# Kernel tuning notes

Hardware: AMD Instinct MI355X
Metric: run time of the kernel (lower is better)

The kernel has to match this reference:

```python
import jax, jax.numpy as jnp
import numpy as np

IN_F = 4096      # in_features (d_model)
OUT_F = 16384    # out_features (4*d_model FFN)
N_TOK = 8192     # tokens = batch*seq
K = OUT_F // 2   # number of kept output rows (static for jit)


def setup_inputs() -> dict:
    key = jax.random.key(0)
    k1, k2, k3, k4 = jax.random.split(key, 4)
    data = jax.random.normal(k1, (N_TOK, IN_F), jnp.float32)
    weight = jax.random.normal(k2, (OUT_F, IN_F), jnp.float32) * 0.02
    bias = jax.random.normal(k3, (OUT_F,), jnp.float32) * 0.02
    # mask with exactly K ones at random positions (static count -> jit-safe)
    perm = jax.random.permutation(k4, OUT_F)
    mask = jnp.zeros((OUT_F,), jnp.int32).at[perm[:K]].set(1)
    return {"data": data, "weight": weight, "bias": bias, "mask": mask}


def reference(data, weight, bias, mask):
    # mask.nonzero()[0] -> selected output-feature indices (ascending, as torch)
    idx = jnp.nonzero(mask, size=K)[0]                 # [K]
    w_sel = jnp.take(weight, idx, axis=0)              # [K, IN_F] row gather
    b_sel = jnp.take(bias, idx, axis=0)                # [K]
    # F.linear: data @ w_sel^T + b_sel  -> [N_TOK, K]
    return jnp.einsum('ti,ki->tk', data, w_sel) + b_sel
```

## Files before the change

kernel.cpp:

```cpp
#include <hip/hip_runtime.h>
#include <hip/hip_bf16.h>

typedef __bf16 bf16_t;
typedef __attribute__((ext_vector_type(8))) __bf16 bf16x8;
typedef __attribute__((ext_vector_type(4))) float f32x4;

constexpr int IN_F  = 4096;
constexpr int OUT_F = 16384;
constexpr int N_TOK = 8192;
constexpr int KSEL  = 8192;
constexpr long A_ELEMS = (long)N_TOK * IN_F;

constexpr int BM = 256, BN = 256, BK = 64;
constexpr int NT = IN_F / BK;

#define GLOBAL_CAST(p) (const __attribute__((address_space(1))) void*)(p)
#define LDS_CAST(p)    (__attribute__((address_space(3))) void*)(p)

__global__ __launch_bounds__(1024) void build_idx_kernel(
    const int* __restrict__ mask, const float* __restrict__ bias,
    int* __restrict__ idx, float* __restrict__ bsel)
{
    const int t    = threadIdx.x;
    const int lane = t & 63;
    const int wave = t >> 6;
    const int base_i = t * 16;

    int m[16];
    const int4* mp = (const int4*)(mask + base_i);
#pragma unroll
    for (int v = 0; v < 4; ++v) {
        int4 q = mp[v];
        m[v*4+0] = q.x; m[v*4+1] = q.y; m[v*4+2] = q.z; m[v*4+3] = q.w;
    }
    int cnt = 0;
#pragma unroll
    for (int j = 0; j < 16; ++j) cnt += (m[j] != 0) ? 1 : 0;

    int incl = cnt;
#pragma unroll
    for (int d = 1; d < 64; d <<= 1) {
        int o = __shfl_up(incl, (unsigned)d);
        if (lane >= d) incl += o;
    }

    __shared__ int wsum[16];
    __shared__ int wbase[16];
    if (lane == 63) wsum[wave] = incl;
    __syncthreads();
    if (t == 0) {
        int s = 0;
        for (int w = 0; w < 16; ++w) { wbase[w] = s; s += wsum[w]; }
    }
    __syncthreads();

    int p = wbase[wave] + (incl - cnt);
#pragma unroll
    for (int j = 0; j < 16; ++j) {
        if (m[j]) {
            int i = base_i + j;
            idx[p]  = i;
            bsel[p] = bias[i];
            ++p;
        }
    }
}

__global__ __launch_bounds__(256) void convert_kernel(
    const float* __restrict__ A, const float* __restrict__ W,
    const int* __restrict__ idx,
    bf16_t* __restrict__ Ab, bf16_t* __restrict__ Wb)
{
    const long nvecA = A_ELEMS / 8;
    const long total = nvecA * 2;
    const long stride = (long)gridDim.x * blockDim.x;
    for (long v = (long)blockIdx.x * blockDim.x + threadIdx.x; v < total; v += stride) {
        const float4* src;
        bf16_t* dst;
        if (v < nvecA) {
            src = (const float4*)(A + v * 8);
            dst = Ab + v * 8;
        } else {
            long u = v - nvecA;
            int j = (int)(u >> 9);
            int k = (int)(u & 511) * 8;
            src = (const float4*)(W + (long)idx[j] * IN_F + k);
            dst = Wb + u * 8;
        }
        float4 x = src[0], y = src[1];
        bf16x8 o;
        o[0]=(bf16_t)x.x; o[1]=(bf16_t)x.y; o[2]=(bf16_t)x.z; o[3]=(bf16_t)x.w;
        o[4]=(bf16_t)y.x; o[5]=(bf16_t)y.y; o[6]=(bf16_t)y.z; o[7]=(bf16_t)y.w;
        *(bf16x8*)dst = o;
    }
}

__global__ __launch_bounds__(512, 2) void gemm8p_kernel(
    const bf16_t* __restrict__ A, const bf16_t* __restrict__ B,
    const float* __restrict__ bsel, float* __restrict__ C)
{
    __shared__ __attribute__((aligned(16))) char lds[131072];

    const int tid  = threadIdx.x;
    const int w    = tid >> 6;
    const int lane = tid & 63;
    const int wr   = w >> 2;
    const int wc   = w & 3;

    const int bid = blockIdx.x;
    const int swz = (bid & 7) * 128 + (bid >> 3);
    const int m0 = (swz & 31) * BM;
    const int n0 = (swz >> 5) * BN;

    const int pr  = lane >> 3;
    const int csw = ((lane & 7) ^ pr) * 8;
    const bf16_t* aSrc[2][2];
    const bf16_t* bSrc[2][2];
#pragma unroll
    for (int h = 0; h < 2; ++h)
#pragma unroll
        for (int j = 0; j < 2; ++j) {
            const int row = h * 128 + (w * 2 + j) * 8 + pr;
            aSrc[h][j] = A + (long)(m0 + row) * IN_F + csw;
            bSrc[h][j] = B + (long)(n0 + row) * IN_F + csw;
        }

#define ST_A(buf, h, tl) do {                                                  \
    __builtin_amdgcn_global_load_lds(GLOBAL_CAST(aSrc[h][0] + (long)(tl)*BK),  \
        LDS_CAST(lds + (buf)*65536 + (h)*16384 + w*2048), 16, 0, 0);           \
    __builtin_amdgcn_global_load_lds(GLOBAL_CAST(aSrc[h][1] + (long)(tl)*BK),  \
        LDS_CAST(lds + (buf)*65536 + (h)*16384 + w*2048 + 1024), 16, 0, 0);    \
} while (0)
#define ST_B(buf, h, tl) do {                                                  \
    __builtin_amdgcn_global_load_lds(GLOBAL_CAST(bSrc[h][0] + (long)(tl)*BK),  \
        LDS_CAST(lds + (buf)*65536 + 32768 + (h)*16384 + w*2048), 16, 0, 0);   \
    __builtin_amdgcn_global_load_lds(GLOBAL_CAST(bSrc[h][1] + (long)(tl)*BK),  \
        LDS_CAST(lds + (buf)*65536 + 32768 + (h)*16384 + w*2048 + 1024),       \
        16, 0, 0);                                                             \
} while (0)

    f32x4 acc[8][4];
#pragma unroll
    for (int m = 0; m < 8; ++m)
#pragma unroll
        for (int n = 0; n < 4; ++n)
#pragma unroll
            for (int j = 0; j < 4; ++j) acc[m][n][j] = 0.f;

    const int fr    = lane & 15;
    const int kslot = lane >> 4;
    const int sp0b = ((kslot       ^ (fr & 7)) << 4);
    const int sp1b = (((4 + kslot) ^ (fr & 7)) << 4);

    const int a0s0 = wr * 16384 + fr * 128 + sp0b;
    const int a0s1 = wr * 16384 + fr * 128 + sp1b;
    const int a1s0 = a0s0 + 65536;
    const int a1s1 = a0s1 + 65536;
    const int bbase = 32768 + (wc >> 1) * 16384 + ((wc & 1) * 64 + fr) * 128;
    const int b0s0 = bbase + sp0b;
    const int b0s1 = bbase + sp1b;
    const int b1s0 = b0s0 + 65536;
    const int b1s1 = b0s1 + 65536;

    bf16x8 af[4][2], bg[4][2];

#define RDA(s0, s1, mq) do {                                                   \
    _Pragma("unroll") for (int mm = 0; mm < 4; ++mm) {                         \
        af[mm][0] = *(const bf16x8*)(lds + (s0) + (mq)*8192 + mm*2048);        \
        af[mm][1] = *(const bf16x8*)(lds + (s1) + (mq)*8192 + mm*2048);        \
    } } while (0)
#define RDB(s0, s1, nh) do {                                                   \
    _Pragma("unroll") for (int nn = 0; nn < 2; ++nn) {                         \
        bg[(nh)*2+nn][0] = *(const bf16x8*)(lds + (s0) + ((nh)*2+nn)*2048);    \
        bg[(nh)*2+nn][1] = *(const bf16x8*)(lds + (s1) + ((nh)*2+nn)*2048);    \
    } } while (0)
#define MFMAQ(mq, nh) do {                                                     \
    __builtin_amdgcn_s_setprio(1);                                             \
    _Pragma("unroll") for (int mm = 0; mm < 4; ++mm)                           \
    _Pragma("unroll") for (int nn = 0; nn < 2; ++nn) {                         \
        const int m = (mq) * 4 + mm, n = (nh) * 2 + nn;                        \
        acc[m][n] = __builtin_amdgcn_mfma_f32_16x16x32_bf16(                   \
            af[mm][0], bg[n][0], acc[m][n], 0, 0, 0);                          \
        acc[m][n] = __builtin_amdgcn_mfma_f32_16x16x32_bf16(                   \
            af[mm][1], bg[n][1], acc[m][n], 0, 0, 0);                          \
    }                                                                          \
    __builtin_amdgcn_s_setprio(0); } while (0)
#define BAR()    __builtin_amdgcn_s_barrier()
#define LGKM0()  asm volatile("s_waitcnt lgkmcnt(0)" ::: "memory")
#define LGKMH()  asm volatile("s_waitcnt lgkmcnt(8)" ::: "memory")
#define VMC8()   asm volatile("s_waitcnt vmcnt(8)" ::: "memory")
#define VMC0()   asm volatile("s_waitcnt vmcnt(0)" ::: "memory")

    ST_A(0, 0, 0); ST_A(0, 1, 0); ST_B(0, 0, 0); ST_B(0, 1, 0);
    ST_A(1, 0, 1); ST_A(1, 1, 1); ST_B(1, 0, 1); ST_B(1, 1, 1);
    VMC8(); BAR();

    for (int I = 0; I < NT / 2; ++I) {
        const int t = 2 * I, u = t + 1;
        const bool s2 = (I < NT / 2 - 1);

        RDA(a0s0, a0s1, 0); RDB(b0s0, b0s1, 0);
        LGKMH(); BAR(); LGKM0(); MFMAQ(0, 0); BAR();
        RDB(b0s0, b0s1, 1);
        BAR(); LGKM0(); MFMAQ(0, 1); BAR();
        RDA(a0s0, a0s1, 1);
        if (s2) { ST_B(0, 0, t + 2); ST_B(0, 1, t + 2); }
        BAR(); LGKM0(); MFMAQ(1, 0); BAR();
        if (s2) { ST_A(0, 0, t + 2); ST_A(0, 1, t + 2); }
        BAR(); MFMAQ(1, 1); if (s2) VMC8(); else VMC0(); BAR();
        RDA(a1s0, a1s1, 0); RDB(b1s0, b1s1, 0);
        LGKMH(); BAR(); LGKM0(); MFMAQ(0, 0); BAR();
        RDB(b1s0, b1s1, 1);
        BAR(); LGKM0(); MFMAQ(0, 1); BAR();
        RDA(a1s0, a1s1, 1);
        if (s2) { ST_B(1, 0, u + 2); ST_B(1, 1, u + 2); }
        BAR(); LGKM0(); MFMAQ(1, 0); BAR();
        if (s2) { ST_A(1, 0, u + 2); ST_A(1, 1, u + 2); }
        BAR(); MFMAQ(1, 1); if (s2) VMC8(); else VMC0(); BAR();
    }
    VMC0();

#undef ST_A
#undef ST_B
#undef RDA
#undef RDB
#undef MFMAQ
#undef BAR
#undef LGKM0
#undef LGKMH
#undef VMC8
#undef VMC0

    float b4[4];
#pragma unroll
    for (int n = 0; n < 4; ++n) b4[n] = bsel[n0 + wc * 64 + n * 16 + fr];

    const int rbase = m0 + wr * 128 + kslot * 4;
#pragma unroll
    for (int m = 0; m < 8; ++m)
#pragma unroll
        for (int n = 0; n < 4; ++n) {
            const int col = n0 + wc * 64 + n * 16 + fr;
#pragma unroll
            for (int j = 0; j < 4; ++j)
                C[(long)(rbase + m * 16 + j) * KSEL + col] = acc[m][n][j] + b4[n];
        }
}

__global__ __launch_bounds__(256) void gemm_f32staged_kernel(
    const float* __restrict__ A, const float* __restrict__ W,
    const int* __restrict__ idx, const float* __restrict__ bsel,
    float* __restrict__ C)
{
    constexpr int FBM = 128, FBN = 128, BK2 = 32;
    __shared__ __attribute__((aligned(16))) float Asf[FBM * BK2];
    __shared__ __attribute__((aligned(16))) float Bsf[FBN * BK2];

    const int tid  = threadIdx.x;
    const int wave = tid >> 6;
    const int lane = tid & 63;
    const int wrf  = wave >> 1;
    const int wcf  = wave & 1;

    const int m0 = blockIdx.x * FBM;
    const int n0 = blockIdx.y * FBN;

    const int srow = lane >> 3;
    const int scol = (lane & 7) * 4;

    const float* aptr[4];
    const float* bptr[4];
#pragma unroll
    for (int i = 0; i < 4; ++i) {
        aptr[i] = A + (long)(m0 + wave * 32 + i * 8 + srow) * IN_F + scol;
        const int br = idx[n0 + wave * 32 + i * 8 + srow];
        bptr[i] = W + (long)br * IN_F + scol;
    }

    f32x4 acc[4][4];
#pragma unroll
    for (int m = 0; m < 4; ++m)
#pragma unroll
        for (int n = 0; n < 4; ++n)
#pragma unroll
            for (int j = 0; j < 4; ++j) acc[m][n][j] = 0.f;

    const int fr = lane & 15;
    const int fk = (lane >> 4) * 8;

    for (int k0 = 0; k0 < IN_F; k0 += BK2) {
#pragma unroll
        for (int i = 0; i < 4; ++i) {
            __builtin_amdgcn_global_load_lds(GLOBAL_CAST(aptr[i] + k0),
                LDS_CAST(&Asf[(wave * 32 + i * 8) * BK2]), 16, 0, 0);
            __builtin_amdgcn_global_load_lds(GLOBAL_CAST(bptr[i] + k0),
                LDS_CAST(&Bsf[(wave * 32 + i * 8) * BK2]), 16, 0, 0);
        }
        __syncthreads();

        bf16x8 af[4], bg[4];
#pragma unroll
        for (int m = 0; m < 4; ++m) {
            const float* p = &Asf[(wrf * 64 + m * 16 + fr) * BK2 + fk];
            f32x4 x = *(const f32x4*)p, y = *(const f32x4*)(p + 4);
#pragma unroll
            for (int j = 0; j < 4; ++j) { af[m][j] = (bf16_t)x[j]; af[m][4+j] = (bf16_t)y[j]; }
        }
#pragma unroll
        for (int n = 0; n < 4; ++n) {
            const float* p = &Bsf[(wcf * 64 + n * 16 + fr) * BK2 + fk];
            f32x4 x = *(const f32x4*)p, y = *(const f32x4*)(p + 4);
#pragma unroll
            for (int j = 0; j < 4; ++j) { bg[n][j] = (bf16_t)x[j]; bg[n][4+j] = (bf16_t)y[j]; }
        }
#pragma unroll
        for (int m = 0; m < 4; ++m)
#pragma unroll
            for (int n = 0; n < 4; ++n)
                acc[m][n] = __builtin_amdgcn_mfma_f32_16x16x32_bf16(
                    af[m], bg[n], acc[m][n], 0, 0, 0);
        __syncthreads();
    }

    float b4[4];
#pragma unroll
    for (int n = 0; n < 4; ++n) b4[n] = bsel[n0 + wcf * 64 + n * 16 + fr];

    const int rbase = m0 + wrf * 64 + (lane >> 4) * 4;
#pragma unroll
    for (int m = 0; m < 4; ++m)
#pragma unroll
        for (int n = 0; n < 4; ++n) {
            const int col = n0 + wcf * 64 + n * 16 + fr;
#pragma unroll
            for (int j = 0; j < 4; ++j)
                C[(long)(rbase + m * 16 + j) * KSEL + col] = acc[m][n][j] + b4[n];
        }
}

extern "C" void kernel_launch(void* const* d_in, const int* in_sizes, int n_in,
                              void* d_out, int out_size, void* d_ws, size_t ws_size,
                              hipStream_t stream)
{
    const float* data   = (const float*)d_in[0];
    const float* weight = (const float*)d_in[1];
    const float* bias   = (const float*)d_in[2];
    const int*   mask   = (const int*)d_in[3];
    float*       out    = (float*)d_out;

    char* ws = (char*)d_ws;
    int*   idx  = (int*)ws;
    float* bsel = (float*)(ws + (KSEL * 4));
    bf16_t* Ab  = (bf16_t*)(ws + (KSEL * 8));
    bf16_t* Wb  = Ab + A_ELEMS;

    const size_t NEED = (size_t)KSEL * 8 + (size_t)A_ELEMS * 2 * 2;

    build_idx_kernel<<<1, 1024, 0, stream>>>(mask, bias, idx, bsel);

    if (ws_size >= NEED) {
        convert_kernel<<<2048, 256, 0, stream>>>(data, weight, idx, Ab, Wb);
        gemm8p_kernel<<<1024, 512, 0, stream>>>(Ab, Wb, bsel, out);
    } else {
        dim3 grid(N_TOK / 128, KSEL / 128);
        gemm_f32staged_kernel<<<grid, 256, 0, stream>>>(data, weight, idx, bsel, out);
    }
}
```

Baseline: 686.7 us.

## Double-buffer LDS fragment registers to overlap reads with MFMA and halve barriers

Splits the A and B register fragments into two sets so that the LDS reads for the next quarter-tile are issued while MFMAs on the current set run. The number of barriers per k-step drops from about two per quarter to one, and the global-load waits are adjusted to vmcnt(4). Register pressure goes up, which can lower occupancy or cause spills. The reworked wait and barrier ordering also carries a risk of LDS read/write races.

```diff
diff --git a/kernel.cpp b/kernel.cpp
--- a/kernel.cpp
+++ b/kernel.cpp
@@ -156,78 +156,107 @@
     const int a0s1 = wr * 16384 + fr * 128 + sp1b;
     const int a1s0 = a0s0 + 65536;
     const int a1s1 = a0s1 + 65536;
-    const int bbase = 32768 + (wc >> 1) * 16384 + ((wc & 1) * 64 + fr) * 128;
-    const int b0s0 = bbase + sp0b;
-    const int b0s1 = bbase + sp1b;
+    const int bb   = 32768 + (wc >> 1) * 16384 + ((wc & 1) * 64 + fr) * 128;
+    const int b0s0 = bb + sp0b;
+    const int b0s1 = bb + sp1b;
     const int b1s0 = b0s0 + 65536;
     const int b1s1 = b0s1 + 65536;
 
-    bf16x8 af[4][2], bg[4][2];
-
-#define RDA(s0, s1, mq) do {                                                   \
+    bf16x8 afA[4][2], afB[4][2], bg0[2][2], bg1[2][2];
+
+#define RDA_TO(DST, s0, s1, mq) do {                                           \
     _Pragma("unroll") for (int mm = 0; mm < 4; ++mm) {                         \
-        af[mm][0] = *(const bf16x8*)(lds + (s0) + (mq)*8192 + mm*2048);        \
-        af[mm][1] = *(const bf16x8*)(lds + (s1) + (mq)*8192 + mm*2048);        \
+        DST[mm][0] = *(const bf16x8*)(lds + (s0) + (mq)*8192 + mm*2048);       \
+        DST[mm][1] = *(const bf16x8*)(lds + (s1) + (mq)*8192 + mm*2048);       \
     } } while (0)
-#define RDB(s0, s1, nh) do {                                                   \
+#define RDB_TO(DST, s0, s1, nh) do {                                           \
     _Pragma("unroll") for (int nn = 0; nn < 2; ++nn) {                         \
-        bg[(nh)*2+nn][0] = *(const bf16x8*)(lds + (s0) + ((nh)*2+nn)*2048);    \
-        bg[(nh)*2+nn][1] = *(const bf16x8*)(lds + (s1) + ((nh)*2+nn)*2048);    \
+        DST[nn][0] = *(const bf16x8*)(lds + (s0) + ((nh)*2+nn)*2048);          \
+        DST[nn][1] = *(const bf16x8*)(lds + (s1) + ((nh)*2+nn)*2048);          \
     } } while (0)
-#define MFMAQ(mq, nh) do {                                                     \
+#define MFMAP(AF, BG, mq, nh) do {                                             \
     __builtin_amdgcn_s_setprio(1);                                             \
     _Pragma("unroll") for (int mm = 0; mm < 4; ++mm)                           \
     _Pragma("unroll") for (int nn = 0; nn < 2; ++nn) {                         \
         const int m = (mq) * 4 + mm, n = (nh) * 2 + nn;                        \
         acc[m][n] = __builtin_amdgcn_mfma_f32_16x16x32_bf16(                   \
-            af[mm][0], bg[n][0], acc[m][n], 0, 0, 0);                          \
+            AF[mm][0], BG[nn][0], acc[m][n], 0, 0, 0);                         \
         acc[m][n] = __builtin_amdgcn_mfma_f32_16x16x32_bf16(                   \
-            af[mm][1], bg[n][1], acc[m][n], 0, 0, 0);                          \
+            AF[mm][1], BG[nn][1], acc[m][n], 0, 0, 0);                         \
     }                                                                          \
     __builtin_amdgcn_s_setprio(0); } while (0)
 #define BAR()    __builtin_amdgcn_s_barrier()
 #define LGKM0()  asm volatile("s_waitcnt lgkmcnt(0)" ::: "memory")
-#define LGKMH()  asm volatile("s_waitcnt lgkmcnt(8)" ::: "memory")
+#define VMC4()   asm volatile("s_waitcnt vmcnt(4)" ::: "memory")
 #define VMC8()   asm volatile("s_waitcnt vmcnt(8)" ::: "memory")
 #define VMC0()   asm volatile("s_waitcnt vmcnt(0)" ::: "memory")
 
-    ST_A(0, 0, 0); ST_A(0, 1, 0); ST_B(0, 0, 0); ST_B(0, 1, 0);
-    ST_A(1, 0, 1); ST_A(1, 1, 1); ST_B(1, 0, 1); ST_B(1, 1, 1);
+    ST_B(0, 0, 0); ST_B(0, 1, 0); ST_A(0, 0, 0); ST_A(0, 1, 0);
+    ST_B(1, 0, 1); ST_B(1, 1, 1); ST_A(1, 0, 1); ST_A(1, 1, 1);
     VMC8(); BAR();
+    RDA_TO(afA, a0s0, a0s1, 0);
+    RDB_TO(bg0, b0s0, b0s1, 0);
 
     for (int I = 0; I < NT / 2; ++I) {
         const int t = 2 * I, u = t + 1;
         const bool s2 = (I < NT / 2 - 1);
 
-        RDA(a0s0, a0s1, 0); RDB(b0s0, b0s1, 0);
-        LGKMH(); BAR(); LGKM0(); MFMAQ(0, 0); BAR();
-        RDB(b0s0, b0s1, 1);
-        BAR(); LGKM0(); MFMAQ(0, 1); BAR();
-        RDA(a0s0, a0s1, 1);
+        LGKM0();
+        RDB_TO(bg1, b0s0, b0s1, 1);
+        MFMAP(afA, bg0, 0, 0);
+        BAR();
+
+        LGKM0();
+        RDA_TO(afB, a0s0, a0s1, 1);
+        MFMAP(afA, bg1, 0, 1);
+        BAR();
+
         if (s2) { ST_B(0, 0, t + 2); ST_B(0, 1, t + 2); }
-        BAR(); LGKM0(); MFMAQ(1, 0); BAR();
+        LGKM0();
+        MFMAP(afB, bg0, 1, 0);
+        if (s2) VMC4(); else VMC0();
+        BAR();
+
         if (s2) { ST_A(0, 0, t + 2); ST_A(0, 1, t + 2); }
-        BAR(); MFMAQ(1, 1); if (s2) VMC8(); else VMC0(); BAR();
-        RDA(a1s0, a1s1, 0); RDB(b1s0, b1s1, 0);
-        LGKMH(); BAR(); LGKM0(); MFMAQ(0, 0); BAR();
-        RDB(b1s0, b1s1, 1);
-        BAR(); LGKM0(); MFMAQ(0, 1); BAR();
-        RDA(a1s0, a1s1, 1);
+        RDA_TO(afA, a1s0, a1s1, 0);
+        RDB_TO(bg0, b1s0, b1s1, 0);
+        MFMAP(afB, bg1, 1, 1);
+        BAR();
+
+        LGKM0();
+        RDB_TO(bg1, b1s0, b1s1, 1);
+        MFMAP(afA, bg0, 0, 0);
+        BAR();
+
+        LGKM0();
+        RDA_TO(afB, a1s0, a1s1, 1);
+        MFMAP(afA, bg1, 0, 1);
+        BAR();
+
         if (s2) { ST_B(1, 0, u + 2); ST_B(1, 1, u + 2); }
-        BAR(); LGKM0(); MFMAQ(1, 0); BAR();
-        if (s2) { ST_A(1, 0, u + 2); ST_A(1, 1, u + 2); }
-        BAR(); MFMAQ(1, 1); if (s2) VMC8(); else VMC0(); BAR();
+        LGKM0();
+        MFMAP(afB, bg0, 1, 0);
+        if (s2) VMC4();
+        BAR();
+
+        if (s2) {
+            ST_A(1, 0, u + 2); ST_A(1, 1, u + 2);
+            RDA_TO(afA, a0s0, a0s1, 0);
+            RDB_TO(bg0, b0s0, b0s1, 0);
+        }
+        MFMAP(afB, bg1, 1, 1);
+        BAR();
     }
     VMC0();
 
 #undef ST_A
 #undef ST_B
-#undef RDA
-#undef RDB
-#undef MFMAQ
+#undef RDA_TO
+#undef RDB_TO
+#undef MFMAP
 #undef BAR
 #undef LGKM0
-#undef LGKMH
+#undef VMC4
 #undef VMC8
 #undef VMC0
 
```

Result: slower. 1.046 ms (+52.4%).
